# Kernel tuning notes

Hardware: AMD Instinct MI355X
Metric: run time of the kernel (lower is better)

The kernel has to match this reference:

```python
import jax, jax.numpy as jnp
import numpy as np
from jax import lax

DIM = 256
QK = 256
HEADS = 8
NWIN = 7
TOPK = 4
KS = 5
SCALE = QK ** (-0.5)


def setup_inputs() -> dict:
    key = jax.random.key(0)
    ks = jax.random.split(key, 5)
    N, H, W = 8, 56, 56
    x = jax.random.normal(ks[0], (N, H, W, DIM), jnp.float32)
    W_qkv = jax.random.normal(ks[1], (DIM, QK + QK + DIM), jnp.float32) * 0.02
    b_qkv = jnp.zeros((QK + QK + DIM,), jnp.float32)
    lepe_w = jax.random.normal(ks[2], (DIM, 1, KS, KS), jnp.float32) * 0.05  # OIHW depthwise
    lepe_b = jnp.zeros((DIM,), jnp.float32)
    W_o = jax.random.normal(ks[3], (DIM, DIM), jnp.float32) * 0.02
    b_o = jnp.zeros((DIM,), jnp.float32)
    return {"x": x, "W_qkv": W_qkv, "b_qkv": b_qkv, "lepe_w": lepe_w,
            "lepe_b": lepe_b, "W_o": W_o, "b_o": b_o}


def reference(x, W_qkv, b_qkv, lepe_w, lepe_b, W_o, b_o):
    N, H, Wd, C = x.shape
    j = i = NWIN
    h, w = H // j, Wd // i
    p2, w2 = j * i, h * w
    hd, hdv = QK // HEADS, DIM // HEADS

    # window partition: n (j h) (i w) c -> n (j i) h w c
    xw = x.reshape(N, j, h, i, w, C).transpose(0, 1, 3, 2, 4, 5).reshape(N, p2, h, w, C)

    qkv = xw @ W_qkv + b_qkv                       # [N, p2, h, w, 2*QK+DIM... actually QK+(QK+DIM)]
    q = qkv[..., :QK]                              # [N, p2, h, w, QK]
    kv = qkv[..., QK:]                             # [N, p2, h, w, QK+DIM]

    q_pix = q.reshape(N, p2, w2, QK)
    kv_pix = kv.reshape(N, p2, w2, QK + DIM)       # identity kv_down

    q_win = q.mean(axis=(2, 3))                    # [N, p2, QK]
    k_win = kv[..., :QK].mean(axis=(2, 3))         # [N, p2, QK]

    # LePE: depthwise conv on v, in image layout
    v_img = kv[..., QK:].reshape(N, j, i, h, w, DIM).transpose(0, 5, 1, 3, 2, 4).reshape(N, DIM, H, Wd)
    pad = KS // 2
    lepe = lax.conv_general_dilated(v_img, lepe_w, (1, 1), [(pad, pad), (pad, pad)],
                                    feature_group_count=DIM)
    lepe = lepe + lepe_b[None, :, None, None]
    lepe = lepe.transpose(0, 2, 3, 1)              # [N, H, W, DIM]

    # coarse routing (detached in original when diff_routing=False)
    qd = lax.stop_gradient(q_win)
    kd = lax.stop_gradient(k_win)
    logit = jnp.einsum('npc,nqc->npq', qd * SCALE, kd)   # [N, p2, p2]
    _, r_idx = lax.top_k(logit, TOPK)              # [N, p2, TOPK]

    # gather top-k windows of kv (mul_weight='none')
    nidx = jnp.arange(N)[:, None, None]
    kv_sel = kv_pix[nidx, r_idx]                   # [N, p2, TOPK, w2, QK+DIM]
    k_sel = kv_sel[..., :QK].reshape(N, p2, TOPK * w2, HEADS, hd).transpose(0, 1, 3, 2, 4)
    v_sel = kv_sel[..., QK:].reshape(N, p2, TOPK * w2, HEADS, hdv).transpose(0, 1, 3, 2, 4)
    qh = q_pix.reshape(N, p2, w2, HEADS, hd).transpose(0, 1, 3, 2, 4)

    attn = jax.nn.softmax(jnp.einsum('npmwc,npmkc->npmwk', qh * SCALE, k_sel), axis=-1)
    out = jnp.einsum('npmwk,npmkc->npmwc', attn, v_sel)  # [N, p2, HEADS, w2, hdv]

    # back to image: (n p2) m (h w) c -> n (j h) (i w) (m c)
    out = out.transpose(0, 1, 3, 2, 4).reshape(N, j, i, h, w, DIM)
    out = out.transpose(0, 1, 3, 2, 4, 5).reshape(N, H, Wd, DIM)

    out = out + lepe
    out = out @ W_o + b_o
    return out
```

## Files before the change

kernel.cpp:

```cpp
#include <hip/hip_runtime.h>
#include <math.h>

#define NBATCH 8
#define HWDIM  56
#define NWIN   7
#define P2     49
#define HEADS  8
#define TOPK   4
#define SCALE  0.0625f
#define NPIX   (NBATCH*HWDIM*HWDIM)

typedef __attribute__((ext_vector_type(8))) short bf16x8;
typedef __attribute__((ext_vector_type(4))) float f32x4;

__device__ __forceinline__ unsigned short f2bf(float f) {
  unsigned u = __float_as_uint(f);
  u += 0x7FFF + ((u >> 16) & 1);
  return (unsigned short)(u >> 16);
}
__device__ __forceinline__ float bf2f(unsigned short h) {
  return __uint_as_float(((unsigned)h) << 16);
}

__global__ __launch_bounds__(256) void convert_x(
    const float* __restrict__ xin, unsigned short* __restrict__ xb)
{
  const int i = (blockIdx.x * 256 + threadIdx.x) * 8;
  float4 a = *(const float4*)&xin[i];
  float4 b = *(const float4*)&xin[i + 4];
  ushort4 o0 = { f2bf(a.x), f2bf(a.y), f2bf(a.z), f2bf(a.w) };
  ushort4 o1 = { f2bf(b.x), f2bf(b.y), f2bf(b.z), f2bf(b.w) };
  *(ushort4*)&xb[i] = o0;
  *(ushort4*)&xb[i + 4] = o1;
}

__global__ __launch_bounds__(256) void prep_w(
    const float* __restrict__ W_qkv, const float* __restrict__ b_qkv,
    const float* __restrict__ W_o, const float* __restrict__ lepe_w,
    unsigned short* __restrict__ Wt_qkv, unsigned short* __restrict__ Wt_o,
    float* __restrict__ b_s, float* __restrict__ Wc)
{
  const int idx = blockIdx.x * 256 + threadIdx.x;
  if (idx < 768 * 256) {
    const int nn = idx >> 8, cc = idx & 255;
    float v = W_qkv[cc * 768 + nn];
    if (nn < 256) v *= SCALE;
    Wt_qkv[idx] = f2bf(v);
  } else if (idx < 768 * 256 + 256 * 256) {
    const int j = idx - 768 * 256;
    const int nn = j >> 8, cc = j & 255;
    Wt_o[j] = f2bf(W_o[cc * 256 + nn]);
  } else if (idx < 768 * 256 + 256 * 256 + 768) {
    const int j = idx - (768 * 256 + 256 * 256);
    b_s[j] = b_qkv[j] * (j < 256 ? SCALE : 1.f);
  } else if (idx < 768 * 256 + 256 * 256 + 768 + 25 * 256) {
    const int j = idx - (768 * 256 + 256 * 256 + 768);
    const int tap = j >> 8, cc = j & 255;
    Wc[j] = lepe_w[cc * 25 + tap];
  }
}

__global__ __launch_bounds__(256) void x_win_kernel(
    const float* __restrict__ x, float* __restrict__ xw)
{
  __shared__ float4 red[256];
  const int bidx = blockIdx.x;
  const int n = bidx / P2, p = bidx - n * P2;
  const int y0 = (p / NWIN) * 8, x0 = (p % NWIN) * 8;
  const int t = threadIdx.x;
  const int c4 = t & 63, pg = t >> 6;
  float4 s = {0.f, 0.f, 0.f, 0.f};
  #pragma unroll
  for (int k = 0; k < 16; ++k) {
    const int pix = pg * 16 + k;
    const int yy = y0 + (pix >> 3), xx = x0 + (pix & 7);
    float4 v = *(const float4*)&x[((size_t)((n * HWDIM + yy) * HWDIM + xx)) * 256 + c4 * 4];
    s.x += v.x; s.y += v.y; s.z += v.z; s.w += v.w;
  }
  red[t] = s;
  __syncthreads();
  if (pg == 0) {
    float4 a = red[c4], b = red[64 + c4], c = red[128 + c4], d = red[192 + c4];
    float4 o = { (a.x + b.x + c.x + d.x) * (1.f/64.f),
                 (a.y + b.y + c.y + d.y) * (1.f/64.f),
                 (a.z + b.z + c.z + d.z) * (1.f/64.f),
                 (a.w + b.w + c.w + d.w) * (1.f/64.f) };
    *(float4*)&xw[(size_t)bidx * 256 + c4 * 4] = o;
  }
}

__global__ __launch_bounds__(256) void win_gemm(
    const float* __restrict__ xw, const float* __restrict__ W_qkv,
    const float* __restrict__ b_qkv,
    float* __restrict__ q_win, float* __restrict__ k_win)
{
  __shared__ float xs[256];
  const int bidx = blockIdx.x;
  const int t = threadIdx.x;
  xs[t] = xw[(size_t)bidx * 256 + t];
  __syncthreads();
  float aq = 0.f, ak = 0.f;
  for (int cc = 0; cc < 256; ++cc) {
    const float xv = xs[cc];
    aq = fmaf(xv, W_qkv[cc * 768 + t], aq);
    ak = fmaf(xv, W_qkv[cc * 768 + 256 + t], ak);
  }
  q_win[(size_t)bidx * 256 + t] = aq + b_qkv[t];
  k_win[(size_t)bidx * 256 + t] = ak + b_qkv[256 + t];
}

__global__ __launch_bounds__(256) void routing_topk(
    const float* __restrict__ q_win, const float* __restrict__ k_win,
    int* __restrict__ r_idx)
{
  __shared__ float qs[256];
  __shared__ float logit[64];
  const int bidx = blockIdx.x;
  const int n = bidx / P2;
  const int t = threadIdx.x;
  qs[t] = q_win[(size_t)bidx * 256 + t];
  __syncthreads();
  const int qq = t >> 2, qt = t & 3;
  if (qq < P2) {
    const float* kb = k_win + ((size_t)(n * P2 + qq)) * 256 + qt * 64;
    float a = 0.f;
    #pragma unroll 8
    for (int i = 0; i < 64; ++i) a = fmaf(qs[qt * 64 + i], kb[i], a);
    a += __shfl_xor(a, 1);
    a += __shfl_xor(a, 2);
    if (qt == 0) logit[qq] = a;
  }
  __syncthreads();
  if (t == 0) {
    float bv0 = -3e38f, bv1 = -3e38f, bv2 = -3e38f, bv3 = -3e38f;
    int bi0 = 0, bi1 = 0, bi2 = 0, bi3 = 0;
    for (int q2 = 0; q2 < P2; ++q2) {
      const float v = logit[q2];
      if (v > bv0) { bv3=bv2; bi3=bi2; bv2=bv1; bi2=bi1; bv1=bv0; bi1=bi0; bv0=v; bi0=q2; }
      else if (v > bv1) { bv3=bv2; bi3=bi2; bv2=bv1; bi2=bi1; bv1=v; bi1=q2; }
      else if (v > bv2) { bv3=bv2; bi3=bi2; bv2=v; bi2=q2; }
      else if (v > bv3) { bv3=v; bi3=q2; }
    }
    int* rp = r_idx + (size_t)bidx * TOPK;
    rp[0] = bi0; rp[1] = bi1; rp[2] = bi2; rp[3] = bi3;
  }
}

template<int MODE>
__global__ __launch_bounds__(256) void gemm_mfma(
    const unsigned short* __restrict__ A,
    const unsigned short* __restrict__ Bt,
    const float* __restrict__ bias,
    unsigned short* __restrict__ C0, unsigned short* __restrict__ C1,
    unsigned short* __restrict__ C2, float* __restrict__ Cf)
{
  __shared__ char smem[32768];
  unsigned short* Asm = (unsigned short*)smem;
  unsigned short* Bsm = (unsigned short*)(smem + 16384);
  float* Cs = (float*)smem;

  const int t = threadIdx.x;
  const int w = t >> 6, l = t & 63;
  const int wr = w >> 1, wc = w & 1;
  const int lr = l & 15, lg = l >> 4;
  const int bm = blockIdx.x, bn = blockIdx.y;
  const int row0 = bm * 128, col0 = bn * 128;

  const f32x4 fzero = {0.f, 0.f, 0.f, 0.f};
  f32x4 acc[4][4];
  #pragma unroll
  for (int m = 0; m < 4; ++m)
    #pragma unroll
    for (int n = 0; n < 4; ++n) acc[m][n] = fzero;

  const int srow = t >> 3, skoff = (t & 7) * 8;
  bf16x8 ra[4], rb[4];
  #pragma unroll
  for (int i = 0; i < 4; ++i) {
    ra[i] = *(const bf16x8*)&A [(size_t)(row0 + i*32 + srow) * 256 + skoff];
    rb[i] = *(const bf16x8*)&Bt[(size_t)(col0 + i*32 + srow) * 256 + skoff];
  }

  for (int step = 0; step < 4; ++step) {
    __syncthreads();
    #pragma unroll
    for (int i = 0; i < 4; ++i) {
      *(bf16x8*)&Asm[(i*32 + srow) * 64 + skoff] = ra[i];
      *(bf16x8*)&Bsm[(i*32 + srow) * 64 + skoff] = rb[i];
    }
    __syncthreads();
    if (step < 3) {
      const int k1 = (step + 1) * 64;
      #pragma unroll
      for (int i = 0; i < 4; ++i) {
        ra[i] = *(const bf16x8*)&A [(size_t)(row0 + i*32 + srow) * 256 + k1 + skoff];
        rb[i] = *(const bf16x8*)&Bt[(size_t)(col0 + i*32 + srow) * 256 + k1 + skoff];
      }
    }
    #pragma unroll
    for (int kk = 0; kk < 2; ++kk) {
      bf16x8 af[4], bb[4];
      #pragma unroll
      for (int m = 0; m < 4; ++m)
        af[m] = *(const bf16x8*)&Asm[(wr*64 + m*16 + lr) * 64 + kk*32 + lg*8];
      #pragma unroll
      for (int n = 0; n < 4; ++n)
        bb[n] = *(const bf16x8*)&Bsm[(wc*64 + n*16 + lr) * 64 + kk*32 + lg*8];
      #pragma unroll
      for (int m = 0; m < 4; ++m)
        #pragma unroll
        for (int n = 0; n < 4; ++n)
          acc[m][n] = __builtin_amdgcn_mfma_f32_16x16x32_bf16(af[m], bb[n], acc[m][n], 0, 0, 0);
    }
  }

  float bcol[4];
  #pragma unroll
  for (int n = 0; n < 4; ++n) bcol[n] = bias[col0 + wc*64 + n*16 + lr];

  #pragma unroll
  for (int hf = 0; hf < 2; ++hf) {
    __syncthreads();
    if (wr == hf) {
      #pragma unroll
      for (int m = 0; m < 4; ++m)
        #pragma unroll
        for (int n = 0; n < 4; ++n)
          #pragma unroll
          for (int r = 0; r < 4; ++r) {
            const int lrow = m*16 + lg*4 + r;
            const int col  = wc*64 + n*16 + lr;
            const int csw  = col ^ ((lrow & 7) << 2);
            Cs[lrow * 128 + csw] = acc[m][n][r] + bcol[n];
          }
    }
    __syncthreads();
    #pragma unroll
    for (int it = 0; it < 8; ++it) {
      const int d = (it * 256 + t) * 4;
      const int lrow = d >> 7;
      const int colL = (d & 127) ^ ((lrow & 7) << 2);
      f32x4 v = *(const f32x4*)&Cs[d];
      const size_t grow = (size_t)(row0 + hf*64 + lrow);
      if (MODE == 0) {
        unsigned short* Cp = (bn < 2) ? C0 : (bn < 4) ? C1 : C2;
        const int lc = (bn & 1) * 128 + colL;
        ushort4 o = { f2bf(v[0]), f2bf(v[1]), f2bf(v[2]), f2bf(v[3]) };
        *(ushort4*)&Cp[grow * 256 + lc] = o;
      } else {
        float4 o = { v[0], v[1], v[2], v[3] };
        *(float4*)&Cf[grow * 256 + (size_t)(bn * 128) + colL] = o;
      }
    }
  }
}

#define KPAD 40
#define PSTR 264

__global__ __launch_bounds__(256) void attn_mfma(
    const unsigned short* __restrict__ q_bf,
    const unsigned short* __restrict__ k_bf,
    const unsigned short* __restrict__ v_bf,
    const int* __restrict__ r_idx,
    unsigned short* __restrict__ o_bf)
{
  __shared__ char smem[76288];
  unsigned short* Ksm = (unsigned short*)smem;
  unsigned short* Vsm = (unsigned short*)(smem + 20480);
  unsigned short* Qsm = (unsigned short*)(smem + 37376);
  unsigned short* Psm = (unsigned short*)(smem + 42496);
  float* Osm = (float*)smem;

  const int b = blockIdx.x;
  const int h = b & 7;
  const int np = b >> 3;
  const int n = np / P2, p = np - n * P2;
  const int t = threadIdx.x;
  const int w = t >> 6, l = t & 63;
  const int lr = l & 15, lg = l >> 4;

  {
    const int wv = r_idx[np * 4 + (t >> 6)];
    const int pix = t & 63;
    const int ky = (wv / NWIN) * 8 + (pix >> 3);
    const int kx = (wv % NWIN) * 8 + (pix & 7);
    const size_t goff = ((size_t)((n * HWDIM + ky) * HWDIM + kx)) * 256 + h * 32;
    #pragma unroll
    for (int j = 0; j < 4; ++j) {
      bf16x8 kv = *(const bf16x8*)&k_bf[goff + j * 8];
      *(bf16x8*)&Ksm[t * KPAD + j * 8] = kv;
      bf16x8 vv = *(const bf16x8*)&v_bf[goff + j * 8];
      #pragma unroll
      for (int e = 0; e < 8; ++e)
        Vsm[(j * 8 + e) * PSTR + t] = (unsigned short)vv[e];
    }
  }
  {
    const int qr = t >> 2, jq = t & 3;
    const int qy = (p / NWIN) * 8 + (qr >> 3);
    const int qx = (p % NWIN) * 8 + (qr & 7);
    *(bf16x8*)&Qsm[qr * KPAD + jq * 8] =
        *(const bf16x8*)&q_bf[((size_t)((n * HWDIM + qy) * HWDIM + qx)) * 256 + h * 32 + jq * 8];
  }
  __syncthreads();

  f32x4 sf[16];
  {
    const f32x4 fzero = {0.f, 0.f, 0.f, 0.f};
    bf16x8 aq = *(const bf16x8*)&Qsm[(w * 16 + lr) * KPAD + lg * 8];
    #pragma unroll
    for (int f = 0; f < 16; ++f) {
      bf16x8 bk = *(const bf16x8*)&Ksm[(f * 16 + lr) * KPAD + lg * 8];
      sf[f] = __builtin_amdgcn_mfma_f32_16x16x32_bf16(aq, bk, fzero, 0, 0, 0);
    }
  }

  float inv[4];
  #pragma unroll
  for (int r = 0; r < 4; ++r) {
    float mx = sf[0][r];
    #pragma unroll
    for (int f = 1; f < 16; ++f) mx = fmaxf(mx, sf[f][r]);
    mx = fmaxf(mx, __shfl_xor(mx, 1));
    mx = fmaxf(mx, __shfl_xor(mx, 2));
    mx = fmaxf(mx, __shfl_xor(mx, 4));
    mx = fmaxf(mx, __shfl_xor(mx, 8));
    float sum = 0.f;
    #pragma unroll
    for (int f = 0; f < 16; ++f) { float e = __expf(sf[f][r] - mx); sf[f][r] = e; sum += e; }
    sum += __shfl_xor(sum, 1);
    sum += __shfl_xor(sum, 2);
    sum += __shfl_xor(sum, 4);
    sum += __shfl_xor(sum, 8);
    inv[r] = 1.f / sum;
  }
  #pragma unroll
  for (int f = 0; f < 16; ++f)
    #pragma unroll
    for (int r = 0; r < 4; ++r) {
      const int q = w * 16 + lg * 4 + r;
      const int key = f * 16 + lr;
      const int blk = (key >> 3) ^ (q & 7);
      Psm[q * PSTR + blk * 8 + (key & 7)] = f2bf(sf[f][r] * inv[r]);
    }
  __syncthreads();

  f32x4 oacc[2];
  oacc[0] = (f32x4){0.f, 0.f, 0.f, 0.f};
  oacc[1] = (f32x4){0.f, 0.f, 0.f, 0.f};
  #pragma unroll
  for (int ks = 0; ks < 8; ++ks) {
    const int ablk = (ks * 4 + lg) ^ (lr & 7);
    bf16x8 ap = *(const bf16x8*)&Psm[(w * 16 + lr) * PSTR + ablk * 8];
    #pragma unroll
    for (int nn = 0; nn < 2; ++nn) {
      bf16x8 bv = *(const bf16x8*)&Vsm[(nn * 16 + lr) * PSTR + ks * 32 + lg * 8];
      oacc[nn] = __builtin_amdgcn_mfma_f32_16x16x32_bf16(ap, bv, oacc[nn], 0, 0, 0);
    }
  }

  #pragma unroll
  for (int nn = 0; nn < 2; ++nn)
    #pragma unroll
    for (int r = 0; r < 4; ++r)
      Osm[(w * 16 + lg * 4 + r) * 36 + nn * 16 + lr] = oacc[nn][r];
  __syncthreads();
  {
    const int q = t >> 2, dq = (t & 3) * 8;
    const int qy = (p / NWIN) * 8 + (q >> 3);
    const int qx = (p % NWIN) * 8 + (q & 7);
    float vo[8];
    #pragma unroll
    for (int e = 0; e < 8; ++e) vo[e] = Osm[q * 36 + dq + e];
    ushort4 o0 = { f2bf(vo[0]), f2bf(vo[1]), f2bf(vo[2]), f2bf(vo[3]) };
    ushort4 o1 = { f2bf(vo[4]), f2bf(vo[5]), f2bf(vo[6]), f2bf(vo[7]) };
    unsigned short* op = &o_bf[((size_t)((n * HWDIM + qy) * HWDIM + qx)) * 256 + h * 32 + dq];
    *(ushort4*)op = o0;
    *(ushort4*)&op[4] = o1;
  }
}

__global__ __launch_bounds__(256) void lepe_add(
    const unsigned short* __restrict__ v_bf, const float* __restrict__ Wc,
    const float* __restrict__ bias, unsigned short* __restrict__ o_bf)
{
  const int gid = blockIdx.x * 256 + threadIdx.x;
  const int c8 = (gid & 31) * 8;
  const int pix = gid >> 5;
  const int n = pix / (HWDIM * HWDIM);
  const int rem = pix - n * (HWDIM * HWDIM);
  const int y = rem / HWDIM, x = rem - y * HWDIM;

  float acc[8];
  {
    float4 b0 = *(const float4*)&bias[c8];
    float4 b1 = *(const float4*)&bias[c8 + 4];
    acc[0]=b0.x; acc[1]=b0.y; acc[2]=b0.z; acc[3]=b0.w;
    acc[4]=b1.x; acc[5]=b1.y; acc[6]=b1.z; acc[7]=b1.w;
  }

  #pragma unroll
  for (int ky = 0; ky < 5; ++ky) {
    const int sy = y + ky - 2;
    if (sy < 0 || sy >= HWDIM) continue;
    #pragma unroll
    for (int kx = 0; kx < 5; ++kx) {
      const int sx = x + kx - 2;
      if (sx < 0 || sx >= HWDIM) continue;
      const bf16x8 vv = *(const bf16x8*)&v_bf[((size_t)((n * HWDIM + sy) * HWDIM + sx)) * 256 + c8];
      const float* wp = &Wc[(ky * 5 + kx) * 256 + c8];
      float4 w0 = *(const float4*)wp;
      float4 w1 = *(const float4*)(wp + 4);
      acc[0] = fmaf(w0.x, bf2f((unsigned short)vv[0]), acc[0]);
      acc[1] = fmaf(w0.y, bf2f((unsigned short)vv[1]), acc[1]);
      acc[2] = fmaf(w0.z, bf2f((unsigned short)vv[2]), acc[2]);
      acc[3] = fmaf(w0.w, bf2f((unsigned short)vv[3]), acc[3]);
      acc[4] = fmaf(w1.x, bf2f((unsigned short)vv[4]), acc[4]);
      acc[5] = fmaf(w1.y, bf2f((unsigned short)vv[5]), acc[5]);
      acc[6] = fmaf(w1.z, bf2f((unsigned short)vv[6]), acc[6]);
      acc[7] = fmaf(w1.w, bf2f((unsigned short)vv[7]), acc[7]);
    }
  }

  unsigned short* op = &o_bf[(size_t)pix * 256 + c8];
  const bf16x8 ov = *(const bf16x8*)op;
  ushort4 o0 = { f2bf(bf2f((unsigned short)ov[0]) + acc[0]),
                 f2bf(bf2f((unsigned short)ov[1]) + acc[1]),
                 f2bf(bf2f((unsigned short)ov[2]) + acc[2]),
                 f2bf(bf2f((unsigned short)ov[3]) + acc[3]) };
  ushort4 o1 = { f2bf(bf2f((unsigned short)ov[4]) + acc[4]),
                 f2bf(bf2f((unsigned short)ov[5]) + acc[5]),
                 f2bf(bf2f((unsigned short)ov[6]) + acc[6]),
                 f2bf(bf2f((unsigned short)ov[7]) + acc[7]) };
  *(ushort4*)op = o0;
  *(ushort4*)(op + 4) = o1;
}

extern "C" void kernel_launch(void* const* d_in, const int* in_sizes, int n_in,
                              void* d_out, int out_size, void* d_ws, size_t ws_size,
                              hipStream_t stream)
{
  const float* x      = (const float*)d_in[0];
  const float* W_qkv  = (const float*)d_in[1];
  const float* b_qkv  = (const float*)d_in[2];
  const float* lepe_w = (const float*)d_in[3];
  const float* lepe_b = (const float*)d_in[4];
  const float* W_o    = (const float*)d_in[5];
  const float* b_o    = (const float*)d_in[6];
  float* out = (float*)d_out;

  char* ws = (char*)d_ws;
  const size_t IMG = (size_t)NPIX * 256;
  unsigned short* x_bf    = (unsigned short*)(ws);
  unsigned short* q_bf    = (unsigned short*)(ws + 2*IMG);
  unsigned short* k_bf    = (unsigned short*)(ws + 4*IMG);
  unsigned short* v_bf    = (unsigned short*)(ws + 6*IMG);
  unsigned short* attn_bf = (unsigned short*)(ws + 8*IMG);
  unsigned short* Wt_qkv  = (unsigned short*)(ws + 10*IMG);
  unsigned short* Wt_o    = (unsigned short*)(ws + 10*IMG + 393216);
  float*          b_s     = (float*)         (ws + 10*IMG + 393216 + 131072);
  float*          x_win   = (float*)         (ws + 10*IMG + 393216 + 131072 + 4096);
  float*          q_win   = x_win + (size_t)NBATCH * P2 * 256;
  float*          k_win   = q_win + (size_t)NBATCH * P2 * 256;
  int*            ridx    = (int*)(k_win + (size_t)NBATCH * P2 * 256);
  float*          Wc      = (float*)(ridx + (size_t)NBATCH * P2 * TOPK);

  convert_x<<<3136, 256, 0, stream>>>(x, x_bf);
  prep_w<<<1052, 256, 0, stream>>>(W_qkv, b_qkv, W_o, lepe_w, Wt_qkv, Wt_o, b_s, Wc);
  x_win_kernel<<<NBATCH * P2, 256, 0, stream>>>(x, x_win);
  win_gemm<<<NBATCH * P2, 256, 0, stream>>>(x_win, W_qkv, b_qkv, q_win, k_win);
  routing_topk<<<NBATCH * P2, 256, 0, stream>>>(q_win, k_win, ridx);
  gemm_mfma<0><<<dim3(196, 6), 256, 0, stream>>>(x_bf, Wt_qkv, b_s,
                                                 q_bf, k_bf, v_bf, nullptr);
  attn_mfma<<<NBATCH * P2 * HEADS, 256, 0, stream>>>(q_bf, k_bf, v_bf, ridx, attn_bf);
  lepe_add<<<3136, 256, 0, stream>>>(v_bf, Wc, lepe_b, attn_bf);
  gemm_mfma<1><<<dim3(196, 2), 256, 0, stream>>>(attn_bf, Wt_o, b_o,
                                                 nullptr, nullptr, nullptr, out);
}
```

Before: 238.6 us.

## Use direct global-to-LDS loads in GEMM and attention, transpose QK^T softmax layout

```diff
diff --git a/kernel.cpp b/kernel.cpp
--- a/kernel.cpp
+++ b/kernel.cpp
@@ -1,4 +1,5 @@
 #include <hip/hip_runtime.h>
+#include <hip/hip_bf16.h>
 #include <math.h>
 
 #define NBATCH 8
@@ -13,10 +14,17 @@
 typedef __attribute__((ext_vector_type(8))) short bf16x8;
 typedef __attribute__((ext_vector_type(4))) float f32x4;
 
+#define GLOBAL_AS __attribute__((address_space(1)))
+#define LDS_AS    __attribute__((address_space(3)))
+
+__device__ __forceinline__ void gload16(const unsigned short* g, unsigned short* l) {
+  __builtin_amdgcn_global_load_lds((const GLOBAL_AS unsigned int*)g,
+                                   (LDS_AS unsigned int*)l, 16, 0, 0);
+}
+
 __device__ __forceinline__ unsigned short f2bf(float f) {
-  unsigned u = __float_as_uint(f);
-  u += 0x7FFF + ((u >> 16) & 1);
-  return (unsigned short)(u >> 16);
+  __hip_bfloat16 h = __float2bfloat16(f);
+  return *reinterpret_cast<unsigned short*>(&h);
 }
 __device__ __forceinline__ float bf2f(unsigned short h) {
   return __uint_as_float(((unsigned)h) << 16);
@@ -173,45 +181,33 @@
     #pragma unroll
     for (int n = 0; n < 4; ++n) acc[m][n] = fzero;
 
-  const int srow = t >> 3, skoff = (t & 7) * 8;
-  bf16x8 ra[4], rb[4];
-  #pragma unroll
-  for (int i = 0; i < 4; ++i) {
-    ra[i] = *(const bf16x8*)&A [(size_t)(row0 + i*32 + srow) * 256 + skoff];
-    rb[i] = *(const bf16x8*)&Bt[(size_t)(col0 + i*32 + srow) * 256 + skoff];
-  }
+  const int srow  = t >> 3;
+  const int skoff = ((t & 7) ^ (srow & 7)) * 8;
 
   for (int step = 0; step < 4; ++step) {
+    const int k0 = step * 64;
+    #pragma unroll
+    for (int i = 0; i < 4; ++i) {
+      gload16(&A [(size_t)(row0 + i*32 + srow) * 256 + k0 + skoff], Asm + i*2048 + t*8);
+      gload16(&Bt[(size_t)(col0 + i*32 + srow) * 256 + k0 + skoff], Bsm + i*2048 + t*8);
+    }
     __syncthreads();
-    #pragma unroll
-    for (int i = 0; i < 4; ++i) {
-      *(bf16x8*)&Asm[(i*32 + srow) * 64 + skoff] = ra[i];
-      *(bf16x8*)&Bsm[(i*32 + srow) * 64 + skoff] = rb[i];
-    }
-    __syncthreads();
-    if (step < 3) {
-      const int k1 = (step + 1) * 64;
-      #pragma unroll
-      for (int i = 0; i < 4; ++i) {
-        ra[i] = *(const bf16x8*)&A [(size_t)(row0 + i*32 + srow) * 256 + k1 + skoff];
-        rb[i] = *(const bf16x8*)&Bt[(size_t)(col0 + i*32 + srow) * 256 + k1 + skoff];
-      }
-    }
     #pragma unroll
     for (int kk = 0; kk < 2; ++kk) {
       bf16x8 af[4], bb[4];
       #pragma unroll
       for (int m = 0; m < 4; ++m)
-        af[m] = *(const bf16x8*)&Asm[(wr*64 + m*16 + lr) * 64 + kk*32 + lg*8];
+        af[m] = *(const bf16x8*)&Asm[(wr*64 + m*16 + lr) * 64 + ((kk*4 + lg) ^ (lr & 7)) * 8];
       #pragma unroll
       for (int n = 0; n < 4; ++n)
-        bb[n] = *(const bf16x8*)&Bsm[(wc*64 + n*16 + lr) * 64 + kk*32 + lg*8];
+        bb[n] = *(const bf16x8*)&Bsm[(wc*64 + n*16 + lr) * 64 + ((kk*4 + lg) ^ (lr & 7)) * 8];
       #pragma unroll
       for (int m = 0; m < 4; ++m)
         #pragma unroll
         for (int n = 0; n < 4; ++n)
           acc[m][n] = __builtin_amdgcn_mfma_f32_16x16x32_bf16(af[m], bb[n], acc[m][n], 0, 0, 0);
     }
+    __syncthreads();
   }
 
   float bcol[4];
@@ -220,7 +216,7 @@
 
   #pragma unroll
   for (int hf = 0; hf < 2; ++hf) {
-    __syncthreads();
+    if (hf) __syncthreads();
     if (wr == hf) {
       #pragma unroll
       for (int m = 0; m < 4; ++m)
@@ -255,8 +251,7 @@
   }
 }
 
-#define KPAD 40
-#define PSTR 264
+#define PSTR 272
 
 __global__ __launch_bounds__(256) void attn_mfma(
     const unsigned short* __restrict__ q_bf,
@@ -265,12 +260,13 @@
     const int* __restrict__ r_idx,
     unsigned short* __restrict__ o_bf)
 {
-  __shared__ char smem[76288];
+  __shared__ char smem[52480];
   unsigned short* Ksm = (unsigned short*)smem;
-  unsigned short* Vsm = (unsigned short*)(smem + 20480);
-  unsigned short* Qsm = (unsigned short*)(smem + 37376);
-  unsigned short* Psm = (unsigned short*)(smem + 42496);
-  float* Osm = (float*)smem;
+  unsigned short* Qsm = (unsigned short*)(smem + 16384);
+  unsigned short* Psm = (unsigned short*)smem;
+  unsigned short* Vsm = (unsigned short*)(smem + 34816);
+  float*          Osm = (float*)(smem + 34816);
+  float*          Ls  = (float*)(smem + 52224);
 
   const int b = blockIdx.x;
   const int h = b & 7;
@@ -280,79 +276,84 @@
   const int w = t >> 6, l = t & 63;
   const int lr = l & 15, lg = l >> 4;
 
-  {
-    const int wv = r_idx[np * 4 + (t >> 6)];
-    const int pix = t & 63;
+  const int4 rv = *(const int4*)&r_idx[np * 4];
+
+  {
+    const int pix = t >> 2, ch = t & 3;
+    #pragma unroll
+    for (int i = 0; i < 4; ++i) {
+      const int wv = (&rv.x)[i];
+      const int ky = (wv / NWIN) * 8 + (pix >> 3);
+      const int kx = (wv % NWIN) * 8 + (pix & 7);
+      const size_t goff = ((size_t)((n * HWDIM + ky) * HWDIM + kx)) * 256 + h * 32;
+      gload16(&k_bf[goff + ch * 8], Ksm + i * 2048 + t * 8);
+    }
+    const int qy = (p / NWIN) * 8 + (pix >> 3);
+    const int qx = (p % NWIN) * 8 + (pix & 7);
+    gload16(&q_bf[((size_t)((n * HWDIM + qy) * HWDIM + qx)) * 256 + h * 32 + ch * 8],
+            Qsm + t * 8);
+  }
+  {
+    const int s = t >> 6, pix = t & 63;
+    const int wv = (&rv.x)[s];
     const int ky = (wv / NWIN) * 8 + (pix >> 3);
     const int kx = (wv % NWIN) * 8 + (pix & 7);
     const size_t goff = ((size_t)((n * HWDIM + ky) * HWDIM + kx)) * 256 + h * 32;
     #pragma unroll
     for (int j = 0; j < 4; ++j) {
-      bf16x8 kv = *(const bf16x8*)&k_bf[goff + j * 8];
-      *(bf16x8*)&Ksm[t * KPAD + j * 8] = kv;
       bf16x8 vv = *(const bf16x8*)&v_bf[goff + j * 8];
       #pragma unroll
       for (int e = 0; e < 8; ++e)
         Vsm[(j * 8 + e) * PSTR + t] = (unsigned short)vv[e];
     }
   }
-  {
-    const int qr = t >> 2, jq = t & 3;
-    const int qy = (p / NWIN) * 8 + (qr >> 3);
-    const int qx = (p % NWIN) * 8 + (qr & 7);
-    *(bf16x8*)&Qsm[qr * KPAD + jq * 8] =
-        *(const bf16x8*)&q_bf[((size_t)((n * HWDIM + qy) * HWDIM + qx)) * 256 + h * 32 + jq * 8];
-  }
   __syncthreads();
 
   f32x4 sf[16];
   {
     const f32x4 fzero = {0.f, 0.f, 0.f, 0.f};
-    bf16x8 aq = *(const bf16x8*)&Qsm[(w * 16 + lr) * KPAD + lg * 8];
+    bf16x8 aq = *(const bf16x8*)&Qsm[(w * 16 + lr) * 32 + lg * 8];
     #pragma unroll
     for (int f = 0; f < 16; ++f) {
-      bf16x8 bk = *(const bf16x8*)&Ksm[(f * 16 + lr) * KPAD + lg * 8];
-      sf[f] = __builtin_amdgcn_mfma_f32_16x16x32_bf16(aq, bk, fzero, 0, 0, 0);
-    }
-  }
-
-  float inv[4];
-  #pragma unroll
-  for (int r = 0; r < 4; ++r) {
-    float mx = sf[0][r];
-    #pragma unroll
-    for (int f = 1; f < 16; ++f) mx = fmaxf(mx, sf[f][r]);
-    mx = fmaxf(mx, __shfl_xor(mx, 1));
-    mx = fmaxf(mx, __shfl_xor(mx, 2));
-    mx = fmaxf(mx, __shfl_xor(mx, 4));
-    mx = fmaxf(mx, __shfl_xor(mx, 8));
+      bf16x8 bk = *(const bf16x8*)&Ksm[(f * 16 + lr) * 32 + lg * 8];
+      sf[f] = __builtin_amdgcn_mfma_f32_16x16x32_bf16(bk, aq, fzero, 0, 0, 0);
+    }
+  }
+
+  {
+    float mx = sf[0][0];
+    #pragma unroll
+    for (int f = 0; f < 16; ++f)
+      #pragma unroll
+      for (int r = 0; r < 4; ++r) mx = fmaxf(mx, sf[f][r]);
+    mx = fmaxf(mx, __shfl_xor(mx, 16));
+    mx = fmaxf(mx, __shfl_xor(mx, 32));
     float sum = 0.f;
     #pragma unroll
-    for (int f = 0; f < 16; ++f) { float e = __expf(sf[f][r] - mx); sf[f][r] = e; sum += e; }
-    sum += __shfl_xor(sum, 1);
-    sum += __shfl_xor(sum, 2);
-    sum += __shfl_xor(sum, 4);
-    sum += __shfl_xor(sum, 8);
-    inv[r] = 1.f / sum;
-  }
-  #pragma unroll
-  for (int f = 0; f < 16; ++f)
-    #pragma unroll
-    for (int r = 0; r < 4; ++r) {
-      const int q = w * 16 + lg * 4 + r;
-      const int key = f * 16 + lr;
-      const int blk = (key >> 3) ^ (q & 7);
-      Psm[q * PSTR + blk * 8 + (key & 7)] = f2bf(sf[f][r] * inv[r]);
-    }
-  __syncthreads();
+    for (int f = 0; f < 16; ++f)
+      #pragma unroll
+      for (int r = 0; r < 4; ++r) {
+        float e = __expf(sf[f][r] - mx);
+        sf[f][r] = e; sum += e;
+      }
+    sum += __shfl_xor(sum, 16);
+    sum += __shfl_xor(sum, 32);
+    if (lg == 0) Ls[w * 16 + lr] = 1.f / sum;
+  }
+  __syncthreads();
+
+  #pragma unroll
+  for (int f = 0; f < 16; ++f) {
+    ushort4 pk = { f2bf(sf[f][0]), f2bf(sf[f][1]), f2bf(sf[f][2]), f2bf(sf[f][3]) };
+    *(ushort4*)&Psm[(w * 16 + lr) * PSTR + f * 16 + lg * 4] = pk;
+  }
 
   f32x4 oacc[2];
   oacc[0] = (f32x4){0.f, 0.f, 0.f, 0.f};
   oacc[1] = (f32x4){0.f, 0.f, 0.f, 0.f};
   #pragma unroll
   for (int ks = 0; ks < 8; ++ks) {
-    const int ablk = (ks * 4 + lg) ^ (lr & 7);
-    bf16x8 ap = *(const bf16x8*)&Psm[(w * 16 + lr) * PSTR + ablk * 8];
+    bf16x8 ap = *(const bf16x8*)&Psm[(w * 16 + lr) * PSTR + ks * 32 + lg * 8];
     #pragma unroll
     for (int nn = 0; nn < 2; ++nn) {
       bf16x8 bv = *(const bf16x8*)&Vsm[(nn * 16 + lr) * PSTR + ks * 32 + lg * 8];
@@ -360,11 +361,16 @@
     }
   }
 
+  float inv4[4];
+  #pragma unroll
+  for (int r = 0; r < 4; ++r) inv4[r] = Ls[w * 16 + lg * 4 + r];
+
+  __syncthreads();
   #pragma unroll
   for (int nn = 0; nn < 2; ++nn)
     #pragma unroll
     for (int r = 0; r < 4; ++r)
-      Osm[(w * 16 + lg * 4 + r) * 36 + nn * 16 + lr] = oacc[nn][r];
+      Osm[(w * 16 + lg * 4 + r) * 36 + nn * 16 + lr] = oacc[nn][r] * inv4[r];
   __syncthreads();
   {
     const int q = t >> 2, dq = (t & 3) * 8;
```

After: 219.2 us. 1.09x faster.
